# Performance work log

Measured on AMD Instinct MI355X. Metric: run time of the kernel, lower is better.

The kernel has to match this reference:

```python
import jax, jax.numpy as jnp
import numpy as np

EPS = 1e-08
ITERATIONS = 3


def squash(s):
    # s: [..., d]
    s2 = jnp.sum(s * s, axis=-1, keepdims=True)
    return s2 / (1.0 + s2) * (s / jnp.sqrt(s2 + EPS))


def setup_inputs() -> dict:
    key = jax.random.key(0)
    k1, k2 = jax.random.split(key)
    B, IN_CAPS, OUT_CAPS, IN_D, OUT_D = 256, 1152, 10, 8, 16
    u = jax.random.normal(k1, (B, IN_CAPS, IN_D), dtype=jnp.float32)
    weight = jax.random.normal(k2, (IN_CAPS, OUT_CAPS, IN_D, OUT_D), dtype=jnp.float32)
    return {"u": u, "weight": weight}


def reference(u, weight):
    # u: [B, in_caps, in_d]; weight: [in_caps, out_caps, in_d, out_d]
    u_hat = jnp.einsum('ijnm,bin->bijm', weight, u)  # [B, in_caps, out_caps, out_d]
    B, in_caps, out_caps, _ = u_hat.shape
    b = jnp.zeros((B, in_caps, out_caps), dtype=u.dtype)
    v = None
    for _ in range(ITERATIONS):
        c = jax.nn.softmax(b, axis=1)  # softmax over in_caps (dim=1, faithful to source)
        s = jnp.einsum('bij,bijm->bjm', c, u_hat)  # [B, out_caps, out_d]
        v = squash(s)
        a = jnp.einsum('bjm,bijm->bij', v, u_hat)
        b = b + a
    return v
```

## Files before the change

kernel.cpp:

```cpp
#include <hip/hip_runtime.h>
#include <hip/hip_bf16.h>
#include <math.h>


#define IC 1152
#define OC 10
#define NB 256
#define TILE_DW (IC * 8)

#define NW_DW (IC * OC * 64)
#define NU_DW (NB * IC * 4)
#define WS_NEED ((size_t)(NW_DW + NU_DW) * 4)

typedef float v2f __attribute__((ext_vector_type(2)));
typedef _Float16 h2 __attribute__((ext_vector_type(2)));

#if defined(__has_builtin)
#if __has_builtin(__builtin_amdgcn_fdot2)
#define HAVE_FDOT2 1
#endif
#endif

__device__ __forceinline__ float fdot2f(unsigned w, unsigned uu, float c) {
    h2 a = *(h2*)&w, b = *(h2*)&uu;
#ifdef HAVE_FDOT2
    return __builtin_amdgcn_fdot2(a, b, c, false);
#else
    return c + (float)a.x * (float)b.x + (float)a.y * (float)b.y;
#endif
}
__device__ __forceinline__ v2f h_v2(unsigned w) {
    h2 h = *(h2*)&w;
    v2f r = {(float)h.x, (float)h.y};
    return r;
}
__device__ __forceinline__ unsigned packh2(float a, float b) {
    h2 h = {(_Float16)a, (_Float16)b};
    return *(unsigned*)&h;
}
__device__ __forceinline__ unsigned short pack1(float a) {
    __hip_bfloat16 h = __float2bfloat16(a);
    return *(unsigned short*)&h;
}
__device__ __forceinline__ unsigned h2bits(h2 v) { return *(unsigned*)&v; }
__device__ __forceinline__ h2 h2shfl_add(h2 v, int o) {
    unsigned b = h2bits(v);
    unsigned s = (unsigned)__shfl_xor((int)b, o, 64);
    return v + *(h2*)&s;
}

__global__ void convert_kernel(const float* __restrict__ u,
                               const float* __restrict__ W,
                               unsigned* __restrict__ ws, int do_u) {
    const int tid = blockIdx.x * blockDim.x + threadIdx.x;
    if (tid < NW_DW) {
        const int k = tid & 3, mp = (tid >> 2) & 3, q = (tid >> 4) & 3, ij = tid >> 6;
        const int m = (q << 2) + mp;
        const float* s = W + ((size_t)ij << 7) + m + (k << 5);
        ws[tid] = packh2(s[0], s[16]);
    } else if (do_u) {
        const int e = tid - NW_DW;
        if (e < NU_DW) {
            const int pr = e & 3, bi = e >> 2;
            const float* s = u + ((size_t)bi << 3) + (pr << 1);
            ws[NW_DW + e] = packh2(s[0], s[1]);
        }
    }
}

template<bool UF16>
__global__ __launch_bounds__(1024, 8)
void caps_route_kernel(const float* __restrict__ u,
                       const unsigned* __restrict__ Wh,
                       const unsigned* __restrict__ ug,
                       float* __restrict__ out) {
    extern __shared__ unsigned smem_u[];
    unsigned* uh = smem_u;
    unsigned short* ce = (unsigned short*)(uh + 2 * TILE_DW);
    float* spart = (float*)(ce + 2 * IC);
    unsigned* r0p = (unsigned*)spart;

    const int t    = threadIdx.x;
    const int bx   = blockIdx.x;
    const int lane = t & 63;
    const int wid  = t >> 6;

    int x = bx & 7, sg = bx >> 3;
    int j, p;
    if (sg < 128) { j = x; p = sg; }
    else { int s2 = sg - 128; j = 8 + (x >> 2); p = ((x & 3) << 5) + s2; }
    const int bb = p * 2;

    {
        const int q  = t & 3;
        const int i0 = t >> 2;
        const int pb = (((q >> 1) ^ ((i0 >> 2) & 1)) << 2) + ((q & 1) << 1);
        const float* u0p = u + (size_t)bb * (IC * 8);
        const uint4* ua4 = (const uint4*)ug + (size_t)bb * IC;
        const uint4* ub4 = ua4 + IC;

        h2 sA01 = {0.f, 0.f}, sA23 = {0.f, 0.f};
        h2 sB01 = {0.f, 0.f}, sB23 = {0.f, 0.f};

        auto stage = [&](int i) {
            const uint4* wq4 = (const uint4*)Wh + (((size_t)(i * OC + j) << 2) + q) * 4;
            uint4 Ua, Ub;
            if constexpr (UF16) {
                Ua = ua4[i];
                Ub = ub4[i];
            } else {
                const float4 a0 = *(const float4*)(u0p + i * 8);
                const float4 a1 = *(const float4*)(u0p + i * 8 + 4);
                const float4 b0 = *(const float4*)(u0p + IC * 8 + i * 8);
                const float4 b1 = *(const float4*)(u0p + IC * 8 + i * 8 + 4);
                Ua = make_uint4(packh2(a0.x, a0.y), packh2(a0.z, a0.w),
                                packh2(a1.x, a1.y), packh2(a1.z, a1.w));
                Ub = make_uint4(packh2(b0.x, b0.y), packh2(b0.z, b0.w),
                                packh2(b1.x, b1.y), packh2(b1.z, b1.w));
            }
#define DOT8(acc, wm, Um) \
            acc = fdot2f(wm.x, Um.x, 0.f);  acc = fdot2f(wm.y, Um.y, acc); \
            acc = fdot2f(wm.z, Um.z, acc);  acc = fdot2f(wm.w, Um.w, acc);
            const uint4 w0 = wq4[0], w1 = wq4[1];
            float A0, A1, B0, B1;
            DOT8(A0, w0, Ua) DOT8(A1, w1, Ua)
            DOT8(B0, w0, Ub) DOT8(B1, w1, Ub)
            const unsigned pa01 = packh2(A0, A1), pb01 = packh2(B0, B1);
            const uint4 w2 = wq4[2], w3 = wq4[3];
            float A2, A3, B2, B3;
            DOT8(A2, w2, Ua) DOT8(A3, w3, Ua)
            DOT8(B2, w2, Ub) DOT8(B3, w3, Ub)
            const unsigned pa23 = packh2(A2, A3), pb23 = packh2(B2, B3);
#undef DOT8
            sA01 += *(const h2*)&pa01;  sA23 += *(const h2*)&pa23;
            sB01 += *(const h2*)&pb01;  sB23 += *(const h2*)&pb23;
            const int dst = (i << 3) + pb;
            *(uint2*)&uh[dst]           = make_uint2(pa01, pa23);
            *(uint2*)&uh[TILE_DW + dst] = make_uint2(pb01, pb23);
        };
#pragma unroll
        for (int k = 0; k < 4; ++k) stage(i0 + 256 * k);
        if (i0 < IC - 1024) stage(i0 + 1024);

#pragma unroll
        for (int o = 4; o <= 32; o <<= 1) {
            sA01 = h2shfl_add(sA01, o);  sA23 = h2shfl_add(sA23, o);
            sB01 = h2shfl_add(sB01, o);  sB23 = h2shfl_add(sB23, o);
        }
        if (lane < 4) {
            *(uint2*)&r0p[wid * 8 + (lane << 1)]       = make_uint2(h2bits(sA01), h2bits(sA23));
            *(uint2*)&r0p[128 + wid * 8 + (lane << 1)] = make_uint2(h2bits(sB01), h2bits(sB23));
        }
    }

    __syncthreads();

    const int bt = wid >> 3;
    const int w8 = wid & 7;
    const int rowbase = w8 * 144;
    const unsigned* uhT = uh + bt * TILE_DW;
    unsigned short* ceT = ce + bt * IC;

    const int mqc = lane & 3;
    const int h   = lane >> 2;
    const int pbS = (((mqc >> 1) ^ ((h >> 2) & 1)) << 2) + ((mqc & 1) << 1);
    const bool eB = ((lane >> 2) & 1) != 0;
    const int sA0 = eB ? 2 : 0, sA1 = eB ? 3 : 1;
    const int sB0 = eB ? 0 : 2, sB1 = eB ? 1 : 3;

    float L[3];
#pragma unroll
    for (int k = 0; k < 3; ++k) L[k] = 0.f;
    float se = 0.f;
    float4 vq;

    auto bupdate = [&](const float4 v4) {
        const unsigned p01 = packh2(v4.x, v4.y), p23 = packh2(v4.z, v4.w);
        const unsigned vh0 = __shfl((int)p01, sA0, 4), vh1 = __shfl((int)p23, sA0, 4);
        const unsigned vh2 = __shfl((int)p01, sA1, 4), vh3 = __shfl((int)p23, sA1, 4);
        const unsigned vh4 = __shfl((int)p01, sB0, 4), vh5 = __shfl((int)p23, sB0, 4);
        const unsigned vh6 = __shfl((int)p01, sB1, 4), vh7 = __shfl((int)p23, sB1, 4);
        se = 0.f;
#define BROW(i, Lk) {                                                     \
        const uint4 da = *(const uint4*)&uhT[(i) << 3];                   \
        const uint4 db = *(const uint4*)&uhT[((i) << 3) + 4];             \
        float dpA = fdot2f(da.x, vh0, 0.f);                               \
        dpA = fdot2f(da.y, vh1, dpA);                                     \
        dpA = fdot2f(da.z, vh2, dpA);                                     \
        dpA = fdot2f(da.w, vh3, dpA);                                     \
        float dpB = fdot2f(db.x, vh4, 0.f);                               \
        dpB = fdot2f(db.y, vh5, dpB);                                     \
        dpB = fdot2f(db.z, vh6, dpB);                                     \
        dpB = fdot2f(db.w, vh7, dpB);                                     \
        Lk += dpA + dpB;                                                  \
        const float ev = __expf(Lk);       \
        ceT[i] = pack1(ev);                                               \
        se += ev; }
        BROW(rowbase + lane, L[0])
        BROW(rowbase + lane + 64, L[1])
        if (lane < 16) { BROW(rowbase + 128 + lane, L[2]) }
#undef BROW
#pragma unroll
        for (int o = 32; o >= 1; o >>= 1) se += __shfl_xor(se, o, 64);
    };

    {
        h2 a01 = {0.f, 0.f}, a23 = {0.f, 0.f};
#pragma unroll
        for (int w = 0; w < 16; ++w) {
            const uint2 d = *(const uint2*)&r0p[bt * 128 + w * 8 + (mqc << 1)];
            a01 += *(const h2*)&d.x;
            a23 += *(const h2*)&d.y;
        }
        const float inv = 1.0f / (float)IC;
        const float4 s4 = make_float4((float)a01.x * inv, (float)a01.y * inv,
                                      (float)a23.x * inv, (float)a23.y * inv);
        float p2 = s4.x*s4.x + s4.y*s4.y + s4.z*s4.z + s4.w*s4.w;
        p2 += __shfl_xor(p2, 1, 64);
        p2 += __shfl_xor(p2, 2, 64);
        const float sc = p2 / ((1.0f + p2) * sqrtf(p2 + 1e-8f));
        vq = make_float4(s4.x * sc, s4.y * sc, s4.z * sc, s4.w * sc);
    }
    bupdate(vq);

    for (int r = 1; r < 3; ++r) {
        v2f aA = {0.f, 0.f}, aB = {0.f, 0.f};
#pragma unroll 3
        for (int k = 0; k < 9; ++k) {
            const int i = rowbase + 16 * k + h;
            const uint2 d = *(const uint2*)&uhT[(i << 3) + pbS];
            const float c = __uint_as_float(((unsigned)ceT[i]) << 16);
            const v2f cs = {c, c};
            aA += cs * h_v2(d.x);
            aB += cs * h_v2(d.y);
        }
        float4 acc = make_float4(aA.x, aA.y, aB.x, aB.y);
#pragma unroll
        for (int o = 4; o <= 32; o <<= 1) {
            acc.x += __shfl_xor(acc.x, o, 64); acc.y += __shfl_xor(acc.y, o, 64);
            acc.z += __shfl_xor(acc.z, o, 64); acc.w += __shfl_xor(acc.w, o, 64);
        }
        float* spR = spart + (r & 1) * 320 + bt * 160;
        if (lane < 4) *(float4*)&spR[w8 * 20 + (lane << 2)] = acc;
        else if (lane == 4) spR[w8 * 20 + 16] = se;
        __syncthreads();

        {
            float4 ss = {0.f, 0.f, 0.f, 0.f};
            float sesum = 0.f;
#pragma unroll
            for (int s8 = 0; s8 < 8; ++s8) {
                const float4 qq = *(const float4*)&spR[s8 * 20 + (mqc << 2)];
                ss.x += qq.x; ss.y += qq.y; ss.z += qq.z; ss.w += qq.w;
                sesum += spR[s8 * 20 + 16];
            }
            const float inv = 1.0f / sesum;
            const float4 s4 = make_float4(ss.x * inv, ss.y * inv, ss.z * inv, ss.w * inv);
            float p2 = s4.x*s4.x + s4.y*s4.y + s4.z*s4.z + s4.w*s4.w;
            p2 += __shfl_xor(p2, 1, 64);
            p2 += __shfl_xor(p2, 2, 64);
            const float sc = p2 / ((1.0f + p2) * sqrtf(p2 + 1e-8f));
            vq = make_float4(s4.x * sc, s4.y * sc, s4.z * sc, s4.w * sc);
        }

        if (r == 2) {
            if (w8 == 0 && lane < 4)
                *(float4*)&out[((size_t)(bb + bt) * OC + j) * 16 + (lane << 2)] = vq;
        } else {
            bupdate(vq);
        }
    }
}

extern "C" void kernel_launch(void* const* d_in, const int* in_sizes, int n_in,
                              void* d_out, int out_size, void* d_ws, size_t ws_size,
                              hipStream_t stream) {
    const float* u = (const float*)d_in[0];
    const float* W = (const float*)d_in[1];
    float* out = (float*)d_out;
    unsigned* ws = (unsigned*)d_ws;

    const int do_u = (ws_size >= WS_NEED) ? 1 : 0;
    const int total = NW_DW + (do_u ? NU_DW : 0);
    convert_kernel<<<(total + 255) / 256, 256, 0, stream>>>(u, W, ws, do_u);

    const size_t shmem = (size_t)2 * TILE_DW * 4
                       + (size_t)2 * IC * 2
                       + 640 * 4;
    if (do_u) {
        hipFuncSetAttribute((const void*)caps_route_kernel<true>,
                            hipFuncAttributeMaxDynamicSharedMemorySize, (int)shmem);
        caps_route_kernel<true><<<(NB / 2) * OC, 1024, shmem, stream>>>(u, ws, ws + NW_DW, out);
    } else {
        hipFuncSetAttribute((const void*)caps_route_kernel<false>,
                            hipFuncAttributeMaxDynamicSharedMemorySize, (int)shmem);
        caps_route_kernel<false><<<(NB / 2) * OC, 1024, shmem, stream>>>(u, ws, ws + NW_DW, out);
    }
}
```

Before: 111.7 us.

## Fuse logit update and weighted sum into one pass with max-stabilized softmax

```diff
diff --git a/kernel.cpp b/kernel.cpp
--- a/kernel.cpp
+++ b/kernel.cpp
@@ -38,15 +38,12 @@
     h2 h = {(_Float16)a, (_Float16)b};
     return *(unsigned*)&h;
 }
-__device__ __forceinline__ unsigned short pack1(float a) {
-    __hip_bfloat16 h = __float2bfloat16(a);
-    return *(unsigned short*)&h;
-}
-__device__ __forceinline__ unsigned h2bits(h2 v) { return *(unsigned*)&v; }
-__device__ __forceinline__ h2 h2shfl_add(h2 v, int o) {
-    unsigned b = h2bits(v);
-    unsigned s = (unsigned)__shfl_xor((int)b, o, 64);
-    return v + *(h2*)&s;
+__device__ __forceinline__ unsigned h2u(h2 v) { return *(unsigned*)&v; }
+__device__ __forceinline__ h2 u2h(unsigned v) { return *(h2*)&v; }
+__device__ __forceinline__ h2 hshfl_xor(h2 v, int m) {
+    unsigned b = *(unsigned*)&v;
+    unsigned r = (unsigned)__shfl_xor((int)b, m, 64);
+    return *(h2*)&r;
 }
 
 __global__ void convert_kernel(const float* __restrict__ u,
@@ -75,10 +72,9 @@
                        const unsigned* __restrict__ ug,
                        float* __restrict__ out) {
     extern __shared__ unsigned smem_u[];
-    unsigned* uh = smem_u;
-    unsigned short* ce = (unsigned short*)(uh + 2 * TILE_DW);
-    float* spart = (float*)(ce + 2 * IC);
-    unsigned* r0p = (unsigned*)spart;
+    unsigned* uh   = smem_u;
+    unsigned* r0p  = uh + 2 * TILE_DW;
+    unsigned* spart = r0p + 256;
 
     const int t    = threadIdx.x;
     const int bx   = blockIdx.x;
@@ -88,7 +84,7 @@
     int x = bx & 7, sg = bx >> 3;
     int j, p;
     if (sg < 128) { j = x; p = sg; }
-    else { int s2 = sg - 128; j = 8 + (x >> 2); p = ((x & 3) << 5) + s2; }
+    else { int s2v = sg - 128; j = 8 + (x >> 2); p = ((x & 3) << 5) + s2v; }
     const int bb = p * 2;
 
     {
@@ -99,8 +95,8 @@
         const uint4* ua4 = (const uint4*)ug + (size_t)bb * IC;
         const uint4* ub4 = ua4 + IC;
 
-        h2 sA01 = {0.f, 0.f}, sA23 = {0.f, 0.f};
-        h2 sB01 = {0.f, 0.f}, sB23 = {0.f, 0.f};
+        h2 sA01 = u2h(0u), sA23 = u2h(0u);
+        h2 sB01 = u2h(0u), sB23 = u2h(0u);
 
         auto stage = [&](int i) {
             const uint4* wq4 = (const uint4*)Wh + (((size_t)(i * OC + j) << 2) + q) * 4;
@@ -132,8 +128,8 @@
             DOT8(B2, w2, Ub) DOT8(B3, w3, Ub)
             const unsigned pa23 = packh2(A2, A3), pb23 = packh2(B2, B3);
 #undef DOT8
-            sA01 += *(const h2*)&pa01;  sA23 += *(const h2*)&pa23;
-            sB01 += *(const h2*)&pb01;  sB23 += *(const h2*)&pb23;
+            sA01 += u2h(pa01);  sA23 += u2h(pa23);
+            sB01 += u2h(pb01);  sB23 += u2h(pb23);
             const int dst = (i << 3) + pb;
             *(uint2*)&uh[dst]           = make_uint2(pa01, pa23);
             *(uint2*)&uh[TILE_DW + dst] = make_uint2(pb01, pb23);
@@ -144,12 +140,12 @@
 
 #pragma unroll
         for (int o = 4; o <= 32; o <<= 1) {
-            sA01 = h2shfl_add(sA01, o);  sA23 = h2shfl_add(sA23, o);
-            sB01 = h2shfl_add(sB01, o);  sB23 = h2shfl_add(sB23, o);
+            sA01 += hshfl_xor(sA01, o);  sA23 += hshfl_xor(sA23, o);
+            sB01 += hshfl_xor(sB01, o);  sB23 += hshfl_xor(sB23, o);
         }
         if (lane < 4) {
-            *(uint2*)&r0p[wid * 8 + (lane << 1)]       = make_uint2(h2bits(sA01), h2bits(sA23));
-            *(uint2*)&r0p[128 + wid * 8 + (lane << 1)] = make_uint2(h2bits(sB01), h2bits(sB23));
+            *(uint2*)&r0p[wid * 8 + (lane << 1)]       = make_uint2(h2u(sA01), h2u(sA23));
+            *(uint2*)&r0p[128 + wid * 8 + (lane << 1)] = make_uint2(h2u(sB01), h2u(sB23));
         }
     }
 
@@ -159,116 +155,135 @@
     const int w8 = wid & 7;
     const int rowbase = w8 * 144;
     const unsigned* uhT = uh + bt * TILE_DW;
-    unsigned short* ceT = ce + bt * IC;
-
-    const int mqc = lane & 3;
-    const int h   = lane >> 2;
-    const int pbS = (((mqc >> 1) ^ ((h >> 2) & 1)) << 2) + ((mqc & 1) << 1);
-    const bool eB = ((lane >> 2) & 1) != 0;
-    const int sA0 = eB ? 2 : 0, sA1 = eB ? 3 : 1;
-    const int sB0 = eB ? 0 : 2, sB1 = eB ? 1 : 3;
-
-    float L[3];
-#pragma unroll
-    for (int k = 0; k < 3; ++k) L[k] = 0.f;
-    float se = 0.f;
-    float4 vq;
-
-    auto bupdate = [&](const float4 v4) {
-        const unsigned p01 = packh2(v4.x, v4.y), p23 = packh2(v4.z, v4.w);
-        const unsigned vh0 = __shfl((int)p01, sA0, 4), vh1 = __shfl((int)p23, sA0, 4);
-        const unsigned vh2 = __shfl((int)p01, sA1, 4), vh3 = __shfl((int)p23, sA1, 4);
-        const unsigned vh4 = __shfl((int)p01, sB0, 4), vh5 = __shfl((int)p23, sB0, 4);
-        const unsigned vh6 = __shfl((int)p01, sB1, 4), vh7 = __shfl((int)p23, sB1, 4);
-        se = 0.f;
-#define BROW(i, Lk) {                                                     \
-        const uint4 da = *(const uint4*)&uhT[(i) << 3];                   \
-        const uint4 db = *(const uint4*)&uhT[((i) << 3) + 4];             \
-        float dpA = fdot2f(da.x, vh0, 0.f);                               \
-        dpA = fdot2f(da.y, vh1, dpA);                                     \
-        dpA = fdot2f(da.z, vh2, dpA);                                     \
-        dpA = fdot2f(da.w, vh3, dpA);                                     \
-        float dpB = fdot2f(db.x, vh4, 0.f);                               \
-        dpB = fdot2f(db.y, vh5, dpB);                                     \
-        dpB = fdot2f(db.z, vh6, dpB);                                     \
-        dpB = fdot2f(db.w, vh7, dpB);                                     \
-        Lk += dpA + dpB;                                                  \
-        const float ev = __expf(Lk);       \
-        ceT[i] = pack1(ev);                                               \
-        se += ev; }
-        BROW(rowbase + lane, L[0])
-        BROW(rowbase + lane + 64, L[1])
-        if (lane < 16) { BROW(rowbase + 128 + lane, L[2]) }
-#undef BROW
-#pragma unroll
-        for (int o = 32; o >= 1; o >>= 1) se += __shfl_xor(se, o, 64);
-    };
-
-    {
-        h2 a01 = {0.f, 0.f}, a23 = {0.f, 0.f};
-#pragma unroll
-        for (int w = 0; w < 16; ++w) {
-            const uint2 d = *(const uint2*)&r0p[bt * 128 + w * 8 + (mqc << 1)];
-            a01 += *(const h2*)&d.x;
-            a23 += *(const h2*)&d.y;
-        }
-        const float inv = 1.0f / (float)IC;
-        const float4 s4 = make_float4((float)a01.x * inv, (float)a01.y * inv,
-                                      (float)a23.x * inv, (float)a23.y * inv);
-        float p2 = s4.x*s4.x + s4.y*s4.y + s4.z*s4.z + s4.w*s4.w;
+
+    const int cp = lane & 7;
+    const int eB = (lane >> 2) & 1;
+    const int i1 = rowbase + lane, i2 = i1 + 64, i3 = rowbase + 128 + lane;
+
+    float L0 = 0.f, L1 = 0.f, L2 = (lane < 16) ? 0.f : -1e30f;
+
+    for (int r = 0; r < 3; ++r) {
+        if (r == 2 && w8 != 0) break;
+
+        float sx, sy;
+        {
+            v2f s2 = {0.f, 0.f};
+            float inv;
+            if (r == 0) {
+                h2 a2 = u2h(0u);
+#pragma unroll
+                for (int w = 0; w < 16; ++w)
+                    a2 += u2h(r0p[bt * 128 + w * 8 + cp]);
+                s2.x = (float)a2.x; s2.y = (float)a2.y;
+                inv = 1.0f / (float)IC;
+            } else {
+                const int base = ((r - 1) & 1) * 160;
+                float ses = 0.f;
+#pragma unroll
+                for (int w = 0; w < 8; ++w) {
+                    const unsigned pw = spart[base + bt * 64 + w * 8 + cp];
+                    const float2 mse = *(const float2*)&spart[base + 128 + (bt * 8 + w) * 2];
+                    const float fac = __expf(mse.x);
+                    const v2f pv = h_v2(pw);
+                    s2.x += pv.x * fac;  s2.y += pv.y * fac;
+                    ses += mse.y * fac;
+                }
+                inv = 1.0f / ses;
+            }
+            sx = s2.x * inv;  sy = s2.y * inv;
+        }
+        float p2 = sx * sx + sy * sy;
         p2 += __shfl_xor(p2, 1, 64);
         p2 += __shfl_xor(p2, 2, 64);
+        p2 += __shfl_xor(p2, 4, 64);
         const float sc = p2 / ((1.0f + p2) * sqrtf(p2 + 1e-8f));
-        vq = make_float4(s4.x * sc, s4.y * sc, s4.z * sc, s4.w * sc);
-    }
-    bupdate(vq);
-
-    for (int r = 1; r < 3; ++r) {
-        v2f aA = {0.f, 0.f}, aB = {0.f, 0.f};
-#pragma unroll 3
-        for (int k = 0; k < 9; ++k) {
-            const int i = rowbase + 16 * k + h;
-            const uint2 d = *(const uint2*)&uhT[(i << 3) + pbS];
-            const float c = __uint_as_float(((unsigned)ceT[i]) << 16);
-            const v2f cs = {c, c};
-            aA += cs * h_v2(d.x);
-            aB += cs * h_v2(d.y);
-        }
-        float4 acc = make_float4(aA.x, aA.y, aB.x, aB.y);
-#pragma unroll
-        for (int o = 4; o <= 32; o <<= 1) {
-            acc.x += __shfl_xor(acc.x, o, 64); acc.y += __shfl_xor(acc.y, o, 64);
-            acc.z += __shfl_xor(acc.z, o, 64); acc.w += __shfl_xor(acc.w, o, 64);
-        }
-        float* spR = spart + (r & 1) * 320 + bt * 160;
-        if (lane < 4) *(float4*)&spR[w8 * 20 + (lane << 2)] = acc;
-        else if (lane == 4) spR[w8 * 20 + 16] = se;
+        const float vx = sx * sc, vy = sy * sc;
+
+        if (r == 2) {
+            if (lane < 8)
+                *(float2*)&out[((size_t)(bb + bt) * OC + j) * 16 + (cp << 1)] =
+                    make_float2(vx, vy);
+            break;
+        }
+
+        const unsigned pk = packh2(vx, vy);
+        unsigned vh[8];
+        const int ebase = eB << 2;
+#pragma unroll
+        for (int k = 0; k < 8; ++k)
+            vh[k] = (unsigned)__shfl((int)pk, k ^ ebase, 8);
+
+#define DP8(Lk, ii) { \
+        const uint4 da = *(const uint4*)&uhT[(ii) << 3]; \
+        const uint4 db = *(const uint4*)&uhT[((ii) << 3) + 4]; \
+        float d1 = fdot2f(da.x, vh[0], 0.f); d1 = fdot2f(da.y, vh[1], d1); \
+        d1 = fdot2f(da.z, vh[2], d1); d1 = fdot2f(da.w, vh[3], d1); \
+        float d2 = fdot2f(db.x, vh[4], 0.f); d2 = fdot2f(db.y, vh[5], d2); \
+        d2 = fdot2f(db.z, vh[6], d2); d2 = fdot2f(db.w, vh[7], d2); \
+        (Lk) += d1 + d2; }
+        DP8(L0, i1)
+        DP8(L1, i2)
+        if (lane < 16) { DP8(L2, i3) }
+#undef DP8
+
+        float M = fmaxf(L0, fmaxf(L1, L2));
+#pragma unroll
+        for (int o = 32; o >= 1; o >>= 1)
+            M = fmaxf(M, __shfl_xor(M, o, 64));
+
+        h2 sa[8];
+#pragma unroll
+        for (int k = 0; k < 8; ++k) sa[k] = u2h(0u);
+        float se = 0.f;
+#define ROW2(Lk, ii) { \
+        const uint4 da = *(const uint4*)&uhT[(ii) << 3]; \
+        const uint4 db = *(const uint4*)&uhT[((ii) << 3) + 4]; \
+        const float ev = __expf((Lk) - M); \
+        se += ev; \
+        const h2 eh = u2h(packh2(ev, ev)); \
+        sa[0] += u2h(da.x) * eh;  sa[1] += u2h(da.y) * eh; \
+        sa[2] += u2h(da.z) * eh;  sa[3] += u2h(da.w) * eh; \
+        sa[4] += u2h(db.x) * eh;  sa[5] += u2h(db.y) * eh; \
+        sa[6] += u2h(db.z) * eh;  sa[7] += u2h(db.w) * eh; }
+        ROW2(L0, i1)
+        ROW2(L1, i2)
+        if (lane < 16) { ROW2(L2, i3) }
+#undef ROW2
+#pragma unroll
+        for (int o = 32; o >= 1; o >>= 1)
+            se += __shfl_xor(se, o, 64);
+
+        h2 tt;
+        {
+            const bool s5 = (((lane >> 5) & 1) ^ eB) != 0;
+            const bool b4 = (lane & 16) != 0, b3 = (lane & 8) != 0;
+            h2 tq[4];
+#pragma unroll
+            for (int q = 0; q < 4; ++q) {
+                h2 snd = s5 ? sa[q] : sa[q + 4];
+                tq[q] = (s5 ? sa[q + 4] : sa[q]) + hshfl_xor(snd, 32);
+            }
+            h2 uq[2];
+#pragma unroll
+            for (int q = 0; q < 2; ++q) {
+                h2 snd = b4 ? tq[q] : tq[q + 2];
+                uq[q] = (b4 ? tq[q + 2] : tq[q]) + hshfl_xor(snd, 16);
+            }
+            {
+                h2 snd = b3 ? uq[0] : uq[1];
+                tt = (b3 ? uq[1] : uq[0]) + hshfl_xor(snd, 8);
+            }
+            tt += hshfl_xor(tt, 4);
+            tt += hshfl_xor(tt, 2);
+            tt += hshfl_xor(tt, 1);
+        }
+
+        const int po = (r & 1) * 160;
+        if ((lane & 7) == 0)
+            spart[po + bt * 64 + w8 * 8 + (lane >> 3)] = h2u(tt);
+        if (lane == 1)
+            *(float2*)&spart[po + 128 + (bt * 8 + w8) * 2] = make_float2(M, se);
         __syncthreads();
-
-        {
-            float4 ss = {0.f, 0.f, 0.f, 0.f};
-            float sesum = 0.f;
-#pragma unroll
-            for (int s8 = 0; s8 < 8; ++s8) {
-                const float4 qq = *(const float4*)&spR[s8 * 20 + (mqc << 2)];
-                ss.x += qq.x; ss.y += qq.y; ss.z += qq.z; ss.w += qq.w;
-                sesum += spR[s8 * 20 + 16];
-            }
-            const float inv = 1.0f / sesum;
-            const float4 s4 = make_float4(ss.x * inv, ss.y * inv, ss.z * inv, ss.w * inv);
-            float p2 = s4.x*s4.x + s4.y*s4.y + s4.z*s4.z + s4.w*s4.w;
-            p2 += __shfl_xor(p2, 1, 64);
-            p2 += __shfl_xor(p2, 2, 64);
-            const float sc = p2 / ((1.0f + p2) * sqrtf(p2 + 1e-8f));
-            vq = make_float4(s4.x * sc, s4.y * sc, s4.z * sc, s4.w * sc);
-        }
-
-        if (r == 2) {
-            if (w8 == 0 && lane < 4)
-                *(float4*)&out[((size_t)(bb + bt) * OC + j) * 16 + (lane << 2)] = vq;
-        } else {
-            bupdate(vq);
-        }
     }
 }
 
@@ -284,9 +299,7 @@
     const int total = NW_DW + (do_u ? NU_DW : 0);
     convert_kernel<<<(total + 255) / 256, 256, 0, stream>>>(u, W, ws, do_u);
 
-    const size_t shmem = (size_t)2 * TILE_DW * 4
-                       + (size_t)2 * IC * 2
-                       + 640 * 4;
+    const size_t shmem = (size_t)(2 * TILE_DW + 256 + 320) * 4;
     if (do_u) {
         hipFuncSetAttribute((const void*)caps_route_kernel<true>,
                             hipFuncAttributeMaxDynamicSharedMemorySize, (int)shmem);
```

Result: faster. 108.7 us (-2.6%).
